# Kernel tuning notes

Measured on AMD Instinct MI355X. Metric: run time of the kernel, lower is better.

The kernel has to match this reference:

```python
import jax, jax.numpy as jnp
import numpy as np

B, S, L, D = 16, 1024, 512, 1024
H = 8
DH = D // H
WD = 256          # word/type embedding dim
VOCAB = 1000      # type vocab
NEG = -1e30


def setup_inputs() -> dict:
    key = jax.random.key(0)
    ks = jax.random.split(key, 16)
    inv = 1.0 / np.sqrt(D)
    return {
        "encoder_outs": jax.random.normal(ks[0], (B, S, D), dtype=jnp.float32),
        "to_sem": jax.random.randint(ks[1], (B, L), 0, S, dtype=jnp.int64),
        "to_sem_type": jax.random.randint(ks[2], (B, L), 0, VOCAB, dtype=jnp.int64),
        "sem_syn": jax.random.randint(ks[3], (B, S), 0, L + 1, dtype=jnp.int64),
        "wq": jax.random.normal(ks[4], (D, D), dtype=jnp.float32) * inv,
        "bq": jnp.zeros((D,), dtype=jnp.float32),
        "wk": jax.random.normal(ks[5], (D, D), dtype=jnp.float32) * inv,
        "bk": jnp.zeros((D,), dtype=jnp.float32),
        "wv": jax.random.normal(ks[6], (D, D), dtype=jnp.float32) * inv,
        "bv": jnp.zeros((D,), dtype=jnp.float32),
        "wo": jax.random.normal(ks[7], (D, D), dtype=jnp.float32) * inv,
        "bo": jnp.zeros((D,), dtype=jnp.float32),
        "type_emb": jax.random.normal(ks[8], (VOCAB, WD), dtype=jnp.float32),
        "w_proj": jax.random.normal(ks[9], (D, D + WD), dtype=jnp.float32) / np.sqrt(D + WD),
        "b_proj": jnp.zeros((D,), dtype=jnp.float32),
        "bias_root": jax.random.normal(ks[10], (1, 1, D), dtype=jnp.float32),
    }


def _forward(encoder_outs, to_sem, to_sem_type, sem_syn,
             wq, bq, wk, bk, wv, bv, wo, bo,
             type_emb, w_proj, b_proj, bias_root):
    bsz, len_sem = to_sem.shape
    src_len = encoder_outs.shape[1]

    # batch_index_select: gather the encoder states at semantic head positions
    sem_vec = jnp.take_along_axis(encoder_outs, to_sem[:, :, None], axis=1)  # [B,L,D]

    # Vectorized mask build (replaces the Python loop + scatter):
    # buf[b,i,j] = (sem_syn[b,j] == i+1) or (j == to_sem[b,i])
    ids = jnp.arange(1, len_sem + 1, dtype=sem_syn.dtype)
    aligned = sem_syn[:, None, :] == ids[None, :, None]                       # [B,L,S]
    self_pos = jnp.arange(src_len)[None, None, :] == to_sem[:, :, None]       # [B,L,S]
    allow = aligned | self_pos                                                # [B,L,S]

    # fairseq-style MHA: q scaled by head_dim**-0.5, in/out proj with bias
    q = (sem_vec @ wq.T + bq) * (DH ** -0.5)
    k = encoder_outs @ wk.T + bk
    v = encoder_outs @ wv.T + bv
    q = q.reshape(bsz, len_sem, H, DH)
    k = k.reshape(bsz, src_len, H, DH)
    v = v.reshape(bsz, src_len, H, DH)

    scores = jnp.einsum("blhd,bshd->bhls", q, k)                              # [B,H,L,S]
    scores = jnp.where(allow[:, None, :, :], scores, NEG)
    attn = jax.nn.softmax(scores, axis=-1)
    ctx = jnp.einsum("bhls,bshd->blhd", attn, v).reshape(bsz, len_sem, D)
    sem_vec = ctx @ wo.T + bo                                                 # [B,L,D]

    # arg/type embedding + concat + projection
    type_vec = type_emb[to_sem_type]                                          # [B,L,WD]
    embedding = jnp.concatenate([sem_vec, type_vec], axis=-1) @ w_proj.T + b_proj

    root = jnp.broadcast_to(bias_root, (bsz, 1, D))
    return embedding, jnp.concatenate([root, embedding], axis=1)


def reference(encoder_outs, to_sem, to_sem_type, sem_syn,
              wq, bq, wk, bk, wv, bv, wo, bo,
              type_emb, w_proj, b_proj, bias_root):
    return _forward(encoder_outs, to_sem, to_sem_type, sem_syn,
                    wq, bq, wk, bk, wv, bv, wo, bo,
                    type_emb, w_proj, b_proj, bias_root)
```

## Files before the change

kernel.cpp:

```cpp
#include <hip/hip_runtime.h>

typedef unsigned short u16;
typedef unsigned int   u32;
typedef unsigned long long u64;
typedef __bf16 bf16x8 __attribute__((ext_vector_type(8)));
typedef float  f32x4  __attribute__((ext_vector_type(4)));

#define B_  16
#define S_  1024
#define L_  512
#define D_  1024
#define H_  8
#define WD_ 256
#define KP_ (D_ + WD_)

__device__ __forceinline__ u16 f2bf(float f) {
    u32 u = __float_as_uint(f);
    return (u16)((u + 0x7FFFu + ((u >> 16) & 1u)) >> 16);
}
__device__ __forceinline__ float bf2f(u16 h) {
    return __uint_as_float(((u32)h) << 16);
}
__device__ __forceinline__ void gload16(const void* g, void* l) {
    __builtin_amdgcn_global_load_lds(
        (const __attribute__((address_space(1))) u32*)(unsigned long long)(g),
        (__attribute__((address_space(3))) u32*)(unsigned long long)(l),
        16, 0, 0);
}

__global__ __launch_bounds__(256) void prep_k(
    const float* __restrict__ enc,
    const float* __restrict__ wk, const float* __restrict__ wv,
    const float* __restrict__ wq, const float* __restrict__ te,
    const float* __restrict__ bk, const float* __restrict__ bv,
    const float* __restrict__ bq,
    const float* __restrict__ wo, const float* __restrict__ wproj,
    const float* __restrict__ bo, const float* __restrict__ bproj,
    u16* __restrict__ enc_bf, u16* __restrict__ wkvq, u16* __restrict__ te_bf,
    float* __restrict__ bkvq, u16* __restrict__ wot,
    u16* __restrict__ wp1, u16* __restrict__ wfin,
    float* __restrict__ beff, float qs)
{
    __shared__ float tile[64][65];
    const int bid = blockIdx.x;
    if (bid < 16384) {
        const int i = (bid * 256 + threadIdx.x) * 4;
        const float4 v = *(const float4*)(enc + i);
        ushort4 o;
        o.x = f2bf(v.x); o.y = f2bf(v.y); o.z = f2bf(v.z); o.w = f2bf(v.w);
        *(ushort4*)(enc_bf + i) = o;
    } else if (bid < 19456) {
        const int b2 = bid - 16384;
        const int plane = b2 >> 10;
        const int i = ((b2 & 1023) * 256 + threadIdx.x) * 4;
        const float* src = plane == 0 ? wk : (plane == 1 ? wv : wq);
        const float s = plane == 2 ? qs : 1.0f;
        const float4 v = *(const float4*)(src + i);
        ushort4 o;
        o.x = f2bf(v.x * s); o.y = f2bf(v.y * s); o.z = f2bf(v.z * s); o.w = f2bf(v.w * s);
        *(ushort4*)(wkvq + (size_t)plane * 1048576 + i) = o;
    } else if (bid < 19706) {
        const int i = ((bid - 19456) * 256 + threadIdx.x) * 4;
        if (i < 256000) {
            const float4 v = *(const float4*)(te + i);
            ushort4 o;
            o.x = f2bf(v.x); o.y = f2bf(v.y); o.z = f2bf(v.z); o.w = f2bf(v.w);
            *(ushort4*)(te_bf + i) = o;
        }
    } else if (bid < 19709) {
        const int i = (bid - 19706) * 1024 + threadIdx.x * 4;
        #pragma unroll
        for (int j = 0; j < 4; ++j) {
            const int idx = i + j;
            bkvq[idx] = (idx < 1024) ? bk[idx]
                      : (idx < 2048 ? bv[idx - 1024] : bq[idx - 2048] * qs);
        }
    } else if (bid < 19965) {
        const int cid = bid - 19709;
        const int t0 = (cid & 15) * 64;
        const int k0 = (cid >> 4) * 64;
        const int tr = threadIdx.x >> 4;
        const int tc = threadIdx.x & 15;
        #pragma unroll
        for (int i = 0; i < 4; ++i) {
            const int r = tr + i * 16;
            const float4 v = *(const float4*)(wo + (size_t)(t0 + r) * 1024 + k0 + tc * 4);
            tile[r][tc * 4 + 0] = v.x; tile[r][tc * 4 + 1] = v.y;
            tile[r][tc * 4 + 2] = v.z; tile[r][tc * 4 + 3] = v.w;
        }
        __syncthreads();
        #pragma unroll
        for (int i = 0; i < 4; ++i) {
            const int r = tr + i * 16;
            ushort4 o;
            o.x = f2bf(tile[tc * 4 + 0][r]);
            o.y = f2bf(tile[tc * 4 + 1][r]);
            o.z = f2bf(tile[tc * 4 + 2][r]);
            o.w = f2bf(tile[tc * 4 + 3][r]);
            *(ushort4*)(wot + (size_t)(k0 + r) * 1024 + t0 + tc * 4) = o;
        }
    } else if (bid < 21245) {
        const int i = ((bid - 19965) * 256 + threadIdx.x) * 4;
        const int n = i / 1280, c = i % 1280;
        const float4 v = *(const float4*)(wproj + i);
        ushort4 o;
        o.x = f2bf(v.x); o.y = f2bf(v.y); o.z = f2bf(v.z); o.w = f2bf(v.w);
        if (c < 1024) *(ushort4*)(wp1 + (size_t)n * 1024 + c) = o;
        else          *(ushort4*)(wfin + (size_t)n * 1280 + c) = o;
    } else {
        const int w = threadIdx.x >> 6, lane = threadIdx.x & 63;
        const int n = (bid - 21245) * 4 + w;
        const float* row = wproj + (size_t)n * 1280;
        float s = 0.f;
        for (int t = lane; t < 1024; t += 64) s += row[t] * bo[t];
        #pragma unroll
        for (int off = 32; off > 0; off >>= 1) s += __shfl_down(s, off);
        if (lane == 0) beff[n] = bproj[n] + s;
    }
}

template <int NT>
__global__ __launch_bounds__(1024, 4) void mm8_k(
    const u16* __restrict__ A, const u16* __restrict__ W,
    const float* __restrict__ bias,
    u16* __restrict__ o0, u16* __restrict__ o1, u16* __restrict__ o2,
    int K, int ntn)
{
    __shared__ alignas(16) u16 lds[65536];
    const int tid  = threadIdx.x;
    const int w    = tid >> 6;
    const int lane = tid & 63;
    const int l15  = lane & 15;
    const int lk   = lane >> 4;
    const int wr   = w >> 2;
    const int wc   = w & 3;

    const int nwg = gridDim.x;
    const int bid = blockIdx.x;
    const int e   = (bid & 7) * (nwg >> 3) + (bid >> 3);
    const int bm0 = (e / ntn) * 256;
    const int bn0 = (e % ntn) * 256;

    const int kc_l = (lane & 3) ^ ((lane >> 3) & 3);
    const u16* gsrc = (w < 8) ? A : W;
    const int rbase = (w < 8) ? bm0 : bn0;
    size_t src[2];
    #pragma unroll
    for (int i = 0; i < 2; ++i) {
        const int row = (w & 7) * 32 + i * 16 + (lane >> 2);
        src[i] = (size_t)(rbase + row) * K + kc_l * 8;
    }
    const int dstA = ((w < 8) ? 0 : 8192) + (w & 7) * 1024;

#define STAGE(t) { u16* d = lds + ((t) & 3) * 16384 + dstA;            \
    gload16(gsrc + src[0] + (size_t)(t) * 32, d);                      \
    gload16(gsrc + src[1] + (size_t)(t) * 32, d + 512); }

    const int rslot = (lk ^ ((l15 >> 1) & 3)) * 8;
    const int aoff = (wr * 64 + l15) * 32 + rslot;
    const int boff = 8192 + (wc * 64 + l15) * 32 + rslot;

    f32x4 acc[4][4] = {};

    STAGE(0); STAGE(1); STAGE(2);
    asm volatile("s_waitcnt vmcnt(4)" ::: "memory");
    __builtin_amdgcn_sched_barrier(0);
    __builtin_amdgcn_s_barrier();

    for (int t = 0; t < NT; ++t) {
        const u16* sa = lds + (t & 3) * 16384 + aoff;
        const u16* sb = lds + (t & 3) * 16384 + boff;
        bf16x8 af[4], bfr[4];
        #pragma unroll
        for (int nf = 0; nf < 4; ++nf) bfr[nf] = *(const bf16x8*)(sb + nf * 512);
        #pragma unroll
        for (int mf = 0; mf < 4; ++mf) af[mf] = *(const bf16x8*)(sa + mf * 512);
        if (t + 3 < NT) STAGE(t + 3);
        __builtin_amdgcn_s_setprio(1);
        #pragma unroll
        for (int mf = 0; mf < 4; ++mf)
            #pragma unroll
            for (int nf = 0; nf < 4; ++nf)
                acc[mf][nf] = __builtin_amdgcn_mfma_f32_16x16x32_bf16(af[mf], bfr[nf], acc[mf][nf], 0, 0, 0);
        __builtin_amdgcn_s_setprio(0);
        if (t < NT - 3)      { asm volatile("s_waitcnt vmcnt(4)" ::: "memory"); }
        else if (t == NT - 3){ asm volatile("s_waitcnt vmcnt(2)" ::: "memory"); }
        else if (t == NT - 2){ asm volatile("s_waitcnt vmcnt(0)" ::: "memory"); }
        __builtin_amdgcn_sched_barrier(0);
        __builtin_amdgcn_s_barrier();
    }
#undef STAGE

    const int plane = bn0 >> 10;
    u16* outp = plane == 0 ? o0 : (plane == 1 ? o1 : o2);
    const int cip0 = (bn0 & 1023) + wc * 64;
    const int colg = bn0 + wc * 64 + l15;
    float bsv[4];
    #pragma unroll
    for (int nf = 0; nf < 4; ++nf) bsv[nf] = bias[colg + nf * 16];
    const int erow = lane >> 3;
    const int echk = lane & 7;
    u16* wlds = lds + w * 2304;

    #pragma unroll
    for (int mf = 0; mf < 4; ++mf) {
        u16* pat = wlds + (mf & 1) * 1152;
        #pragma unroll
        for (int nf = 0; nf < 4; ++nf) {
            #pragma unroll
            for (int r = 0; r < 4; ++r) {
                const float val = acc[mf][nf][r] + bsv[nf];
                const float pv = __shfl_xor(val, 1, 64);
                if ((l15 & 1) == 0) {
                    const u32 pk = (u32)f2bf(val) | ((u32)f2bf(pv) << 16);
                    *(u32*)(pat + (lk * 4 + r) * 72 + nf * 16 + l15) = pk;
                }
            }
        }
        asm volatile("s_waitcnt lgkmcnt(0)" ::: "memory");
        __builtin_amdgcn_sched_barrier(0);
        #pragma unroll
        for (int j2 = 0; j2 < 2; ++j2) {
            const int rr = j2 * 8 + erow;
            const uint4 vv = *(const uint4*)(pat + rr * 72 + echk * 8);
            const int grow = bm0 + wr * 64 + mf * 16 + rr;
            *(uint4*)(outp + (size_t)grow * 1024 + cip0 + echk * 8) = vv;
        }
    }
}

#define AM_PLAIN  0
#define AM_CONCAT 2
#define OM_BF16   0
#define OM_FINAL  1

template <int NT, int AMODE, int OMODE>
__global__ __launch_bounds__(256) void mm_k(
    const u16* __restrict__ A, const u16* __restrict__ W,
    const float* __restrict__ bias,
    u16* __restrict__ Ybf, float* __restrict__ Yf, float* __restrict__ Y2,
    int K, int ostride,
    const int* __restrict__ gidx, const u16* __restrict__ aux,
    const float* __restrict__ broot)
{
    constexpr int N = 1024;
    __shared__ alignas(16) u16 lds[32768];

    const int bid = blockIdx.x;
    if (OMODE == OM_FINAL && bid >= 512) {
        const int i = (bid - 512) * 256 + threadIdx.x;
        const int b = i >> 10, d = i & 1023;
        Y2[(size_t)b * (L_ + 1) * D_ + d] = broot[d];
        return;
    }

    const int tid  = threadIdx.x;
    const int wid  = tid >> 6;
    const int lane = tid & 63;
    const int l15  = lane & 15;
    const int lk   = lane >> 4;

    const int nwg = (OMODE == OM_FINAL) ? 512 : gridDim.x;
    const int e   = (bid & 7) * (nwg >> 3) + (bid >> 3);
    const int bm0 = (e >> 3) * 128;
    const int bn0 = (e & 7) * 128;

    const int kc_l = (lane & 3) ^ ((lane >> 3) & 3);
    long ga[2], gw[2], gt[2];
    #pragma unroll
    for (int i = 0; i < 2; ++i) {
        const int row = wid * 32 + i * 16 + (lane >> 2);
        if (AMODE == AM_CONCAT) {
            ga[i] = (long)(bm0 + row) * D_ + kc_l * 8;
            gt[i] = (long)gidx[bm0 + row] * WD_ + kc_l * 8;
        } else {
            ga[i] = (long)(bm0 + row) * K + kc_l * 8;
            gt[i] = 0;
        }
        gw[i] = (long)(bn0 + row) * K + kc_l * 8;
    }

#define MSTAGE(t) { const int k0t = (t) * 32;                              \
    u16* d  = lds + ((t) & 3) * 8192 + wid * 1024;                         \
    u16* db = d + 4096;                                                    \
    if (AMODE == AM_CONCAT && k0t >= D_) {                                 \
        gload16(aux + gt[0] + (k0t - D_), d);                              \
        gload16(aux + gt[1] + (k0t - D_), d + 512);                        \
    } else {                                                               \
        gload16(A + ga[0] + k0t, d);                                       \
        gload16(A + ga[1] + k0t, d + 512);                                 \
    }                                                                      \
    gload16(W + gw[0] + k0t, db);                                          \
    gload16(W + gw[1] + k0t, db + 512); }

    f32x4 acc[4][4] = {};

    const int moff = (wid >> 1) * 64;
    const int noff = (wid & 1) * 64;
    const int rslot = (lk ^ ((l15 >> 1) & 3)) * 8;
    const int aoff = (moff + l15) * 32 + rslot;
    const int boff = 4096 + (noff + l15) * 32 + rslot;

    MSTAGE(0); MSTAGE(1); MSTAGE(2);
    asm volatile("s_waitcnt vmcnt(8)" ::: "memory");
    __builtin_amdgcn_sched_barrier(0);
    __builtin_amdgcn_s_barrier();

    for (int t = 0; t < NT; ++t) {
        const u16* sa = lds + (t & 3) * 8192 + aoff;
        const u16* sb = lds + (t & 3) * 8192 + boff;
        bf16x8 af[4], bfr[4];
        #pragma unroll
        for (int j = 0; j < 4; ++j) bfr[j] = *(const bf16x8*)(sb + j * 512);
        #pragma unroll
        for (int i = 0; i < 4; ++i) af[i] = *(const bf16x8*)(sa + i * 512);
        if (t + 3 < NT) MSTAGE(t + 3);
        __builtin_amdgcn_s_setprio(1);
        #pragma unroll
        for (int i = 0; i < 4; ++i)
            #pragma unroll
            for (int j = 0; j < 4; ++j)
                acc[i][j] = __builtin_amdgcn_mfma_f32_16x16x32_bf16(af[i], bfr[j], acc[i][j], 0, 0, 0);
        __builtin_amdgcn_s_setprio(0);
        if (t < NT - 3)      { asm volatile("s_waitcnt vmcnt(8)" ::: "memory"); }
        else if (t == NT - 3){ asm volatile("s_waitcnt vmcnt(4)" ::: "memory"); }
        else if (t == NT - 2){ asm volatile("s_waitcnt vmcnt(0)" ::: "memory"); }
        __builtin_amdgcn_sched_barrier(0);
        __builtin_amdgcn_s_barrier();
    }
#undef MSTAGE

    #pragma unroll
    for (int j = 0; j < 4; ++j) {
        const int col = bn0 + noff + j * 16 + l15;
        const float bj = bias ? bias[col] : 0.f;
        #pragma unroll
        for (int i = 0; i < 4; ++i) {
            const int mrow = bm0 + moff + i * 16 + lk * 4;
            #pragma unroll
            for (int r = 0; r < 4; ++r) {
                const float val = acc[i][j][r] + bj;
                const long m = mrow + r;
                if (OMODE == OM_BF16) {
                    Ybf[m * (long)ostride + col] = f2bf(val);
                } else {
                    Yf[m * (long)N + col] = val;
                    const long bb = m >> 9, ll = m & 511;
                    Y2[((bb * (L_ + 1)) + ll + 1) * (long)D_ + col] = val;
                }
            }
        }
    }
}

__global__ __launch_bounds__(256) void attn_k(
    const u16* __restrict__ kb, const u16* __restrict__ vb,
    const int* __restrict__ sem_syn, const int* __restrict__ to_sem,
    const u16* __restrict__ qf, u16* __restrict__ ctx)
{
    __shared__ int   list[S_];
    __shared__ float sc[H_][S_];
    __shared__ int   wcnt[16];

    const int bl  = blockIdx.x;
    const int b   = bl >> 9;
    const int l   = bl & 511;
    const int tid = threadIdx.x;
    const int wvi = tid >> 6;
    const int ln  = tid & 63;

    const int tosem = to_sem[bl];
    const ushort4 qu = *(const ushort4*)(qf + ((size_t)b * S_ + tosem) * D_ + tid * 4);
    const float4 qv = make_float4(bf2f(qu.x), bf2f(qu.y), bf2f(qu.z), bf2f(qu.w));

    bool al[4];
    #pragma unroll
    for (int j = 0; j < 4; ++j) {
        const int s = tid * 4 + j;
        const int a = sem_syn[b * S_ + s];
        al[j] = (a == l + 1) || (s == tosem);
    }
    u64 msk[4];
    #pragma unroll
    for (int j = 0; j < 4; ++j) msk[j] = __ballot(al[j]);
    if (ln == 0) {
        #pragma unroll
        for (int j = 0; j < 4; ++j) wcnt[wvi * 4 + j] = __popcll(msk[j]);
    }
    __syncthreads();
    int mybase[4];
    {
        int tot = 0;
        #pragma unroll
        for (int i2 = 0; i2 < 16; ++i2) {
            const int c2 = wcnt[i2];
            #pragma unroll
            for (int j2 = 0; j2 < 4; ++j2)
                if (i2 == wvi * 4 + j2) mybase[j2] = tot;
            tot += c2;
        }
    }
    const u64 lmlt = (1ull << ln) - 1ull;
    #pragma unroll
    for (int j = 0; j < 4; ++j)
        if (al[j]) list[mybase[j] + __popcll(msk[j] & lmlt)] = tid * 4 + j;
    int n = 0;
    #pragma unroll
    for (int i2 = 0; i2 < 16; ++i2) n += wcnt[i2];
    __syncthreads();

    const int g = tid >> 5;
    const int lane = tid & 31;
    for (int i = 0; i < n; ++i) {
        const u16* krow = kb + ((size_t)b * S_ + list[i]) * D_;
        const ushort4 ku = *(const ushort4*)(krow + tid * 4);
        float p = bf2f(ku.x) * qv.x + bf2f(ku.y) * qv.y + bf2f(ku.z) * qv.z + bf2f(ku.w) * qv.w;
        #pragma unroll
        for (int off = 16; off > 0; off >>= 1) p += __shfl_down(p, off, 32);
        if (lane == 0) sc[g][i] = p;
    }
    __syncthreads();

    float mx = -3.0e38f;
    for (int i = lane; i < n; i += 32) mx = fmaxf(mx, sc[g][i]);
    #pragma unroll
    for (int off = 16; off > 0; off >>= 1) mx = fmaxf(mx, __shfl_xor(mx, off, 32));
    float sum = 0.f;
    for (int i = lane; i < n; i += 32) {
        const float e = expf(sc[g][i] - mx);
        sc[g][i] = e;
        sum += e;
    }
    #pragma unroll
    for (int off = 16; off > 0; off >>= 1) sum += __shfl_xor(sum, off, 32);
    const float inv = 1.0f / sum;
    __syncthreads();

    float4 a4 = make_float4(0.f, 0.f, 0.f, 0.f);
    for (int i = 0; i < n; ++i) {
        const float wgt = sc[g][i] * inv;
        const u16* vrow = vb + ((size_t)b * S_ + list[i]) * D_;
        const ushort4 vu = *(const ushort4*)(vrow + tid * 4);
        a4.x = fmaf(wgt, bf2f(vu.x), a4.x);
        a4.y = fmaf(wgt, bf2f(vu.y), a4.y);
        a4.z = fmaf(wgt, bf2f(vu.z), a4.z);
        a4.w = fmaf(wgt, bf2f(vu.w), a4.w);
    }
    ushort4 o;
    o.x = f2bf(a4.x); o.y = f2bf(a4.y); o.z = f2bf(a4.z); o.w = f2bf(a4.w);
    *(ushort4*)(ctx + (size_t)bl * D_ + tid * 4) = o;
}

extern "C" void kernel_launch(void* const* d_in, const int* in_sizes, int n_in,
                              void* d_out, int out_size, void* d_ws, size_t ws_size,
                              hipStream_t stream)
{
    const float* enc    = (const float*)d_in[0];
    const int*   to_sem = (const int*)  d_in[1];
    const int*   tstype = (const int*)  d_in[2];
    const int*   semsyn = (const int*)  d_in[3];
    const float* wq = (const float*)d_in[4];
    const float* bq = (const float*)d_in[5];
    const float* wk = (const float*)d_in[6];
    const float* bk = (const float*)d_in[7];
    const float* wv = (const float*)d_in[8];
    const float* bv = (const float*)d_in[9];
    const float* wo = (const float*)d_in[10];
    const float* bo = (const float*)d_in[11];
    const float* temb  = (const float*)d_in[12];
    const float* wproj = (const float*)d_in[13];
    const float* bproj = (const float*)d_in[14];
    const float* broot = (const float*)d_in[15];

    float* out1 = (float*)d_out;
    float* out2 = out1 + (size_t)B_ * L_ * D_;

    unsigned char* ws = (unsigned char*)d_ws;
    u16*   enc_bf = (u16*)(ws);
    u16*   k_bf   = (u16*)(ws + (32ull << 20));
    u16*   wkvq   = (u16*)(ws + (64ull << 20));
    u16*   wot    = (u16*)(ws + (70ull << 20));
    u16*   wp1    = (u16*)(ws + (72ull << 20));
    u16*   wfin   = (u16*)(ws + (74ull << 20));
    float* beff   = (float*)(ws + (77ull << 20));
    float* bkvq   = (float*)(ws + (77ull << 20) + 8192);
    u16*   ctx_bf = (u16*)(ws + (78ull << 20));
    u16*   te_bf  = (u16*)(ws + (94ull << 20));

    u16* v_bf = (u16*)d_out;
    u16* q_bf = (u16*)((unsigned char*)d_out + (32ull << 20));

    const float qscale = 0.08838834764831845f;
    dim3 blk(256);

    prep_k<<<dim3(21501), blk, 0, stream>>>(
        enc, wk, wv, wq, temb, bk, bv, bq, wo, wproj, bo, bproj,
        enc_bf, wkvq, te_bf, bkvq, wot, wp1, wfin, beff, qscale);

    mm8_k<32><<<dim3(768), dim3(1024), 0, stream>>>(
        enc_bf, wkvq, bkvq, k_bf, v_bf, q_bf, 1024, 12);

    mm_k<32, AM_PLAIN, OM_BF16><<<dim3(64), blk, 0, stream>>>(
        wp1, wot, nullptr, wfin, nullptr, nullptr, 1024, 1280, nullptr, nullptr, nullptr);

    attn_k<<<dim3(B_ * L_), blk, 0, stream>>>(k_bf, v_bf, semsyn, to_sem, q_bf, ctx_bf);

    mm_k<40, AM_CONCAT, OM_FINAL><<<dim3(576), blk, 0, stream>>>(
        ctx_bf, wfin, beff, nullptr, out1, out2, KP_, 1024, tstype, te_bf, broot);
}
```

Baseline: 218.5 us.

## Merge weight-fold GEMM into attention kernel as extra blocks

The small 64-block GEMM that folds the output projection into the final projection weights is moved into the attention launch as 64 extra blocks, run alongside the 8192 attention blocks. This removes one kernel launch and lets the weight GEMM overlap with attention instead of occupying the GPU on its own with low occupancy. Shared memory becomes one raw buffer sized for the larger of the two roles, which may change attention-block occupancy. The GEMM blocks have the highest indices, so they may be scheduled last and form a tail.

```diff
diff --git a/kernel.cpp b/kernel.cpp
--- a/kernel.cpp
+++ b/kernel.cpp
@@ -353,23 +353,101 @@
     }
 }
 
-__global__ __launch_bounds__(256) void attn_k(
+__global__ __launch_bounds__(256) void aw_k(
     const u16* __restrict__ kb, const u16* __restrict__ vb,
     const int* __restrict__ sem_syn, const int* __restrict__ to_sem,
-    const u16* __restrict__ qf, u16* __restrict__ ctx)
+    const u16* __restrict__ qf, u16* __restrict__ ctx,
+    const u16* __restrict__ wp1, const u16* __restrict__ wot,
+    u16* __restrict__ wfin)
 {
-    __shared__ int   list[S_];
-    __shared__ float sc[H_][S_];
-    __shared__ int   wcnt[16];
-
-    const int bl  = blockIdx.x;
-    const int b   = bl >> 9;
-    const int l   = bl & 511;
+    __shared__ alignas(16) unsigned char shm[36928];
+    const int bid = blockIdx.x;
     const int tid = threadIdx.x;
+
+    if (bid >= 8192) {
+        u16* lds = (u16*)shm;
+        const int bid2 = bid - 8192;
+        const int wid  = tid >> 6;
+        const int lane = tid & 63;
+        const int l15  = lane & 15;
+        const int lk   = lane >> 4;
+        const int e    = (bid2 & 7) * 8 + (bid2 >> 3);
+        const int bm0  = (e >> 3) * 128;
+        const int bn0  = (e & 7) * 128;
+        const int K    = 1024;
+
+        const int kc_l = (lane & 3) ^ ((lane >> 3) & 3);
+        long ga[2], gw[2];
+        #pragma unroll
+        for (int i = 0; i < 2; ++i) {
+            const int row = wid * 32 + i * 16 + (lane >> 2);
+            ga[i] = (long)(bm0 + row) * K + kc_l * 8;
+            gw[i] = (long)(bn0 + row) * K + kc_l * 8;
+        }
+
+#define WSTAGE(t) { u16* d = lds + ((t) & 1) * 8192 + wid * 1024;      \
+    gload16(wp1 + ga[0] + (size_t)(t) * 32, d);                        \
+    gload16(wp1 + ga[1] + (size_t)(t) * 32, d + 512);                  \
+    gload16(wot + gw[0] + (size_t)(t) * 32, d + 4096);                 \
+    gload16(wot + gw[1] + (size_t)(t) * 32, d + 4608); }
+
+        f32x4 acc[4][4] = {};
+        const int moff = (wid >> 1) * 64;
+        const int noff = (wid & 1) * 64;
+        const int rslot = (lk ^ ((l15 >> 1) & 3)) * 8;
+        const int aoff = (moff + l15) * 32 + rslot;
+        const int boff = 4096 + (noff + l15) * 32 + rslot;
+
+        WSTAGE(0);
+        for (int t = 0; t < 32; ++t) {
+            if (t + 1 < 32) {
+                WSTAGE(t + 1);
+                asm volatile("s_waitcnt vmcnt(4)" ::: "memory");
+            } else {
+                asm volatile("s_waitcnt vmcnt(0)" ::: "memory");
+            }
+            __builtin_amdgcn_sched_barrier(0);
+            __builtin_amdgcn_s_barrier();
+            const u16* sa = lds + (t & 1) * 8192 + aoff;
+            const u16* sb = lds + (t & 1) * 8192 + boff;
+            bf16x8 af[4], bfr[4];
+            #pragma unroll
+            for (int j = 0; j < 4; ++j) bfr[j] = *(const bf16x8*)(sb + j * 512);
+            #pragma unroll
+            for (int i = 0; i < 4; ++i) af[i] = *(const bf16x8*)(sa + i * 512);
+            #pragma unroll
+            for (int i = 0; i < 4; ++i)
+                #pragma unroll
+                for (int j = 0; j < 4; ++j)
+                    acc[i][j] = __builtin_amdgcn_mfma_f32_16x16x32_bf16(af[i], bfr[j], acc[i][j], 0, 0, 0);
+            __builtin_amdgcn_s_barrier();
+        }
+#undef WSTAGE
+
+        #pragma unroll
+        for (int j = 0; j < 4; ++j) {
+            const int col = bn0 + noff + j * 16 + l15;
+            #pragma unroll
+            for (int i = 0; i < 4; ++i) {
+                const int mrow = bm0 + moff + i * 16 + lk * 4;
+                #pragma unroll
+                for (int r = 0; r < 4; ++r)
+                    wfin[(long)(mrow + r) * 1280 + col] = f2bf(acc[i][j][r]);
+            }
+        }
+        return;
+    }
+
+    int*   list = (int*)shm;
+    float* sc   = (float*)(shm + 4096);
+    int*   wcnt = (int*)(shm + 4096 + 32768);
+
+    const int b   = bid >> 9;
+    const int l   = bid & 511;
     const int wvi = tid >> 6;
     const int ln  = tid & 63;
 
-    const int tosem = to_sem[bl];
+    const int tosem = to_sem[bid];
     const ushort4 qu = *(const ushort4*)(qf + ((size_t)b * S_ + tosem) * D_ + tid * 4);
     const float4 qv = make_float4(bf2f(qu.x), bf2f(qu.y), bf2f(qu.z), bf2f(qu.w));
 
@@ -417,18 +495,18 @@
         float p = bf2f(ku.x) * qv.x + bf2f(ku.y) * qv.y + bf2f(ku.z) * qv.z + bf2f(ku.w) * qv.w;
         #pragma unroll
         for (int off = 16; off > 0; off >>= 1) p += __shfl_down(p, off, 32);
-        if (lane == 0) sc[g][i] = p;
+        if (lane == 0) sc[g * 1024 + i] = p;
     }
     __syncthreads();
 
     float mx = -3.0e38f;
-    for (int i = lane; i < n; i += 32) mx = fmaxf(mx, sc[g][i]);
+    for (int i = lane; i < n; i += 32) mx = fmaxf(mx, sc[g * 1024 + i]);
     #pragma unroll
     for (int off = 16; off > 0; off >>= 1) mx = fmaxf(mx, __shfl_xor(mx, off, 32));
     float sum = 0.f;
     for (int i = lane; i < n; i += 32) {
-        const float e = expf(sc[g][i] - mx);
-        sc[g][i] = e;
+        const float e = expf(sc[g * 1024 + i] - mx);
+        sc[g * 1024 + i] = e;
         sum += e;
     }
     #pragma unroll
@@ -438,7 +516,7 @@
 
     float4 a4 = make_float4(0.f, 0.f, 0.f, 0.f);
     for (int i = 0; i < n; ++i) {
-        const float wgt = sc[g][i] * inv;
+        const float wgt = sc[g * 1024 + i] * inv;
         const u16* vrow = vb + ((size_t)b * S_ + list[i]) * D_;
         const ushort4 vu = *(const ushort4*)(vrow + tid * 4);
         a4.x = fmaf(wgt, bf2f(vu.x), a4.x);
@@ -448,7 +526,7 @@
     }
     ushort4 o;
     o.x = f2bf(a4.x); o.y = f2bf(a4.y); o.z = f2bf(a4.z); o.w = f2bf(a4.w);
-    *(ushort4*)(ctx + (size_t)bl * D_ + tid * 4) = o;
+    *(ushort4*)(ctx + (size_t)bid * D_ + tid * 4) = o;
 }
 
 extern "C" void kernel_launch(void* const* d_in, const int* in_sizes, int n_in,
@@ -500,10 +578,8 @@
     mm8_k<32><<<dim3(768), dim3(1024), 0, stream>>>(
         enc_bf, wkvq, bkvq, k_bf, v_bf, q_bf, 1024, 12);
 
-    mm_k<32, AM_PLAIN, OM_BF16><<<dim3(64), blk, 0, stream>>>(
-        wp1, wot, nullptr, wfin, nullptr, nullptr, 1024, 1280, nullptr, nullptr, nullptr);
-
-    attn_k<<<dim3(B_ * L_), blk, 0, stream>>>(k_bf, v_bf, semsyn, to_sem, q_bf, ctx_bf);
+    aw_k<<<dim3(8256), blk, 0, stream>>>(
+        k_bf, v_bf, semsyn, to_sem, q_bf, ctx_bf, wp1, wot, wfin);
 
     mm_k<40, AM_CONCAT, OM_FINAL><<<dim3(576), blk, 0, stream>>>(
         ctx_bf, wfin, beff, nullptr, out1, out2, KP_, 1024, tstype, te_bf, broot);
```

New measurement: 230.7 us. +5.6%, slower.
